# Kernel tuning notes

Hardware: AMD Instinct MI355X
Metric: run time of the kernel (lower is better)

Reference implementation:

```python
import jax, jax.numpy as jnp
import numpy as np

B, L, D, H, O = 512, 256, 256, 128, 256  # batch, max_len, input_dim, hidden_dim, output_dim


def setup_inputs() -> dict:
    key = jax.random.key(0)
    ks = jax.random.split(key, 16)
    s = 0.1
    n = jax.random.normal
    return {
        "sequences": n(ks[0], (B, L, D), jnp.float32),
        "seqlens": jax.random.randint(ks[1], (B,), 1, L + 1, jnp.int32),
        # forward-direction GRU params (PyTorch layout: gates [r, z, n] stacked)
        "Wih_f": s * n(ks[2], (3 * H, D), jnp.float32),
        "Whh_f": s * n(ks[3], (3 * H, H), jnp.float32),
        "bih_f": s * n(ks[4], (3 * H,), jnp.float32),
        "bhh_f": s * n(ks[5], (3 * H,), jnp.float32),
        # backward-direction GRU params
        "Wih_b": s * n(ks[6], (3 * H, D), jnp.float32),
        "Whh_b": s * n(ks[7], (3 * H, H), jnp.float32),
        "bih_b": s * n(ks[8], (3 * H,), jnp.float32),
        "bhh_b": s * n(ks[9], (3 * H,), jnp.float32),
        # attention MLP + context vector
        "W_mlp": s * n(ks[10], (O, 2 * H), jnp.float32),
        "b_mlp": s * n(ks[11], (O,), jnp.float32),
        "ctx": s * n(ks[12], (O,), jnp.float32),
    }


def _gru(xs, mask, Wih, Whh, bih, bhh, reverse):
    """Masked GRU scan. xs: [L,B,D], mask: [L,B,1]. Returns hidden states [L,B,H]."""
    def step(h, inp):
        x_t, m_t = inp
        gx = x_t @ Wih.T + bih          # [B, 3H]
        gh = h @ Whh.T + bhh            # [B, 3H]
        xr, xz, xn = jnp.split(gx, 3, axis=-1)
        hr, hz, hn = jnp.split(gh, 3, axis=-1)
        r = jax.nn.sigmoid(xr + hr)
        z = jax.nn.sigmoid(xz + hz)
        cand = jnp.tanh(xn + r * hn)
        h_new = (1.0 - z) * cand + z * h
        h = jnp.where(m_t, h_new, h)    # hold state on padding steps
        return h, h

    h0 = jnp.zeros((xs.shape[1], Whh.shape[1]), xs.dtype)
    _, hs = jax.lax.scan(step, h0, (xs, mask), reverse=reverse)
    return hs


def reference(sequences, seqlens, Wih_f, Whh_f, bih_f, bhh_f, Wih_b, Whh_b, bih_b, bhh_b, W_mlp, b_mlp, ctx):
    mask = jnp.arange(L)[None, :] < seqlens[:, None]      # [B, L] valid-token mask
    xs = sequences.transpose(1, 0, 2)                      # [L, B, D]
    m = mask.T[:, :, None]                                 # [L, B, 1]
    hf = _gru(xs, m, Wih_f, Whh_f, bih_f, bhh_f, False)    # forward direction
    hb = _gru(xs, m, Wih_b, Whh_b, bih_b, bhh_b, True)     # backward direction
    rnn_out = jnp.concatenate([hf, hb], axis=-1).transpose(1, 0, 2)  # [B, L, 2H]
    mlp_out = jnp.tanh(rnn_out @ W_mlp.T + b_mlp)          # [B, L, O]
    scores = jnp.einsum('blo,o->bl', mlp_out, ctx)         # [B, L]
    neg = jnp.finfo(scores.dtype).min
    w = jax.nn.softmax(jnp.where(mask, scores, neg), axis=1)  # per-sequence softmax over valid positions
    return jnp.einsum('bl,blh->bh', w, rnn_out)            # [B, 2H] attention-pooled embedding
```

## Files before the change

kernel.cpp:

```cpp
#include <hip/hip_runtime.h>
#include <hip/hip_bf16.h>
#include <cstdint>
#include <cstddef>

#define BATCH 512
#define SEQL 256
#define DIN 256
#define HID 128
#define OUTD 256
#define G3 384
#define TCH 64
#define NCH 4
#define NBS 16
#define NGRPS (BATCH/NBS)
#define MTOT (BATCH*SEQL)
#define MCH  (BATCH*TCH)
#define HSPAD 136
#define NGXT 3072

typedef __attribute__((ext_vector_type(8))) short short8v;
typedef __attribute__((ext_vector_type(4))) float float4v;

__device__ __forceinline__ unsigned short f2bf_u(float x) {
  union { float f; uint32_t u; } v; v.f = x;
  uint32_t r = v.u + 0x7FFFu + ((v.u >> 16) & 1u);
  return (unsigned short)(r >> 16);
}
__device__ __forceinline__ float bfu2f(unsigned short u) {
  union { uint32_t u; float f; } v; v.u = ((uint32_t)u) << 16; return v.f;
}
__device__ __forceinline__ float fast_tanh(float x) {
  float e2 = __expf(-2.0f * x);
  return (1.0f - e2) / (1.0f + e2);
}

__global__ __launch_bounds__(256) void prep_split(
    const float* __restrict__ Wm, unsigned short* __restrict__ mhi, unsigned short* __restrict__ mlo,
    const float* __restrict__ Wf, unsigned short* __restrict__ fhi, unsigned short* __restrict__ flo,
    const float* __restrict__ Wb, unsigned short* __restrict__ bhi, unsigned short* __restrict__ blo)
{
  int gid = blockIdx.x * 256 + threadIdx.x;
  const float* src; unsigned short* hi; unsigned short* lo; int off;
  if (gid < 16384)      { src = Wm; hi = mhi; lo = mlo; off = gid * 4; }
  else if (gid < 40960) { src = Wf; hi = fhi; lo = flo; off = (gid - 16384) * 4; }
  else                  { src = Wb; hi = bhi; lo = blo; off = (gid - 40960) * 4; }
  float4 w4 = *(const float4*)&src[off];
  ushort4 h4, l4;
  h4.x = f2bf_u(w4.x); l4.x = f2bf_u(w4.x - bfu2f(h4.x));
  h4.y = f2bf_u(w4.y); l4.y = f2bf_u(w4.y - bfu2f(h4.y));
  h4.z = f2bf_u(w4.z); l4.z = f2bf_u(w4.z - bfu2f(h4.z));
  h4.w = f2bf_u(w4.w); l4.w = f2bf_u(w4.w - bfu2f(h4.w));
  *(ushort4*)&hi[off] = h4;
  *(ushort4*)&lo[off] = l4;
}

__device__ __forceinline__ void gx_tile(
    int tid, int m0, int yy,
    const float* __restrict__ X,
    const unsigned short* __restrict__ WhiF, const unsigned short* __restrict__ WloF,
    const unsigned short* __restrict__ WhiB, const unsigned short* __restrict__ WloB,
    const float* __restrict__ bf, const float* __restrict__ bb,
    unsigned short* __restrict__ bufF, unsigned short* __restrict__ bufB, int cF, int cB,
    unsigned short* Abf, unsigned short* Bhi, unsigned short* Blo)
{
  const unsigned short* Whi; const unsigned short* Wlo;
  const float* bias; unsigned short* buf; int c;
  if (yy < 6) { Whi = WhiF; Wlo = WloF; bias = bf; buf = bufF; c = cF; }
  else        { yy -= 6; Whi = WhiB; Wlo = WloB; bias = bb; buf = bufB; c = cB; }
  const int n0 = yy * 64;

  const int l  = tid & 63;
  const int w  = tid >> 6;
  const int fr = l & 15;
  const int fk = (l >> 4) * 8;

  float4v acc[2][4];
#pragma unroll
  for (int a = 0; a < 2; ++a)
#pragma unroll
    for (int nb = 0; nb < 4; ++nb) acc[a][nb] = (float4v)0.0f;

  for (int k0 = 0; k0 < DIN; k0 += 32) {
#pragma unroll
    for (int j = 0; j < 4; ++j) {
      int row = (tid >> 3) + j * 32;
      int kq  = (tid & 7) * 4;
      int r   = m0 + row;
      int b_  = r >> 6, tt = r & 63;
      int xrow = b_ * SEQL + c * TCH + tt;
      float4 x4 = *(const float4*)&X[(size_t)xrow * DIN + k0 + kq];
      ushort4 h4 = {f2bf_u(x4.x), f2bf_u(x4.y), f2bf_u(x4.z), f2bf_u(x4.w)};
      *(ushort4*)&Abf[row * 40 + kq] = h4;
    }
    {
      int half = tid & 1;
      int cc   = tid >> 1;
      int col  = cc >> 1;
      int seg  = (cc & 1) * 16;
      const unsigned short* srcw = (half ? Wlo : Whi) + (size_t)(n0 + col) * DIN + k0 + seg;
      unsigned short* dst = (half ? Blo : Bhi) + col * 40 + seg;
      *(short8v*)dst       = *(const short8v*)srcw;
      *(short8v*)(dst + 8) = *(const short8v*)(srcw + 8);
    }
    __syncthreads();

    short8v ah[2], bh[4], blv[4];
#pragma unroll
    for (int a = 0; a < 2; ++a)
      ah[a] = *(const short8v*)&Abf[(w * 32 + a * 16 + fr) * 40 + fk];
#pragma unroll
    for (int nb = 0; nb < 4; ++nb) {
      bh[nb]  = *(const short8v*)&Bhi[(nb * 16 + fr) * 40 + fk];
      blv[nb] = *(const short8v*)&Blo[(nb * 16 + fr) * 40 + fk];
    }
#pragma unroll
    for (int a = 0; a < 2; ++a)
#pragma unroll
      for (int nb = 0; nb < 4; ++nb) {
        acc[a][nb] = __builtin_amdgcn_mfma_f32_16x16x32_bf16(ah[a], bh[nb],  acc[a][nb], 0, 0, 0);
        acc[a][nb] = __builtin_amdgcn_mfma_f32_16x16x32_bf16(ah[a], blv[nb], acc[a][nb], 0, 0, 0);
      }
    __syncthreads();
  }

#pragma unroll
  for (int a = 0; a < 2; ++a)
#pragma unroll
    for (int nb = 0; nb < 4; ++nb) {
      int gate = n0 + nb * 16 + fr;
      float bv_ = bias[gate];
#pragma unroll
      for (int reg = 0; reg < 4; ++reg) {
        int r = m0 + w * 32 + a * 16 + (l >> 4) * 4 + reg;
        buf[(size_t)r * G3 + gate] = f2bf_u(acc[a][nb][reg] + bv_);
      }
    }
}

__device__ __forceinline__ void scan_block(
    int sb, int tid,
    const int* __restrict__ seqlens,
    const float* __restrict__ Whh_f, const float* __restrict__ Whh_b,
    const float* __restrict__ bhh_f, const float* __restrict__ bhh_b,
    const unsigned short* __restrict__ bufF, const unsigned short* __restrict__ bufB,
    float* __restrict__ hstate, __hip_bfloat16* __restrict__ rnn, int ci,
    unsigned short (*hsbuf)[NBS * HSPAD])
{
  const int fwd = (sb < NGRPS) ? 1 : 0;
  const int grp = fwd ? sb : (sb - NGRPS);
  const int b0  = grp * NBS;
  const int w   = tid >> 6;
  const int l   = tid & 63;
  const int col = l & 15;
  const int rq  = l >> 4;
  const int hidx = w * 16 + col;
  const float* Whh = fwd ? Whh_f : Whh_b;
  const float* bhh = fwd ? bhh_f : bhh_b;
  const unsigned short* buf = fwd ? bufF : bufB;
  const int c = fwd ? ci : (NCH - 1 - ci);

  short8v Bh[3][4], Bl[3][4];
  float bias_[3];
#pragma unroll
  for (int j = 0; j < 3; ++j) {
    const int g = j * HID + hidx;
    bias_[j] = bhh[g];
#pragma unroll
    for (int ks = 0; ks < 4; ++ks) {
      const float* p = Whh + (size_t)g * HID + ks * 32 + rq * 8;
      float4 x0 = *(const float4*)p;
      float4 x1 = *(const float4*)(p + 4);
      float v[8] = {x0.x, x0.y, x0.z, x0.w, x1.x, x1.y, x1.z, x1.w};
      short8v hi8, lo8;
#pragma unroll
      for (int e = 0; e < 8; ++e) {
        unsigned short h = f2bf_u(v[e]);
        hi8[e] = (short)h;
        lo8[e] = (short)f2bf_u(v[e] - bfu2f(h));
      }
      Bh[j][ks] = hi8; Bl[j][ks] = lo8;
    }
  }

  int len_[4];
#pragma unroll
  for (int reg = 0; reg < 4; ++reg) len_[reg] = seqlens[b0 + rq * 4 + reg];
  int gmax = 0;
  for (int nb = 0; nb < NBS; ++nb) gmax = max(gmax, seqlens[b0 + nb]);

  float* hst = hstate + ((size_t)((fwd ? 0 : 1) * NGRPS + grp)) * (NBS * HID);
  float hold[4];
#pragma unroll
  for (int reg = 0; reg < 4; ++reg) {
    int nb = rq * 4 + reg;
    hold[reg] = (ci == 0) ? 0.0f : hst[nb * HID + hidx];
    hsbuf[0][nb * HSPAD + hidx] = f2bf_u(hold[reg]);
  }
  __syncthreads();

  int nsteps = gmax - c * TCH;
  nsteps = (nsteps > TCH) ? TCH : nsteps;

  float gxc[3][4], gxn[3][4];
  if (nsteps > 0) {
    int tt0 = fwd ? 0 : (nsteps - 1);
#pragma unroll
    for (int j = 0; j < 3; ++j)
#pragma unroll
      for (int reg = 0; reg < 4; ++reg)
        gxc[j][reg] = bfu2f(buf[(size_t)((b0 + rq * 4 + reg) * TCH + tt0) * G3 + j * HID + hidx]);
  }

  int cur = 0;
  for (int ss = 0; ss < nsteps; ++ss) {
    const int tt = fwd ? ss : (nsteps - 1 - ss);
    const int t  = c * TCH + tt;

    short8v ah[4];
#pragma unroll
    for (int ks = 0; ks < 4; ++ks)
      ah[ks] = *(const short8v*)&hsbuf[cur][col * HSPAD + ks * 32 + rq * 8];

    {
      int ssn = (ss + 1 < nsteps) ? (ss + 1) : ss;
      int ttn = fwd ? ssn : (nsteps - 1 - ssn);
#pragma unroll
      for (int j = 0; j < 3; ++j)
#pragma unroll
        for (int reg = 0; reg < 4; ++reg)
          gxn[j][reg] = bfu2f(buf[(size_t)((b0 + rq * 4 + reg) * TCH + ttn) * G3 + j * HID + hidx]);
    }

    float4v acc[3];
#pragma unroll
    for (int j = 0; j < 3; ++j)
      acc[j] = (float4v){bias_[j], bias_[j], bias_[j], bias_[j]};
#pragma unroll
    for (int ks = 0; ks < 4; ++ks) {
#pragma unroll
      for (int j = 0; j < 3; ++j) {
        acc[j] = __builtin_amdgcn_mfma_f32_16x16x32_bf16(ah[ks], Bh[j][ks], acc[j], 0, 0, 0);
        acc[j] = __builtin_amdgcn_mfma_f32_16x16x32_bf16(ah[ks], Bl[j][ks], acc[j], 0, 0, 0);
      }
    }

#pragma unroll
    for (int reg = 0; reg < 4; ++reg) {
      int nb = rq * 4 + reg;
      float gr = acc[0][reg] + gxc[0][reg];
      float gz = acc[1][reg] + gxc[1][reg];
      float gn = acc[2][reg];
      float xn = gxc[2][reg];
      float r = 1.0f / (1.0f + __expf(-gr));
      float z = 1.0f / (1.0f + __expf(-gz));
      float e2 = __expf(-2.0f * (xn + r * gn));
      float cand = (1.0f - e2) / (1.0f + e2);
      float hv = (1.0f - z) * cand + z * hold[reg];
      bool act = (t < len_[reg]);
      hv = act ? hv : hold[reg];
      hold[reg] = hv;
      hsbuf[cur ^ 1][nb * HSPAD + hidx] = f2bf_u(hv);
      if (act)
        rnn[(size_t)((b0 + nb) * SEQL + t) * OUTD + (fwd ? 0 : HID) + hidx] =
            __float2bfloat16(hv);
    }
    asm volatile("s_waitcnt lgkmcnt(0)" ::: "memory");
    __builtin_amdgcn_s_barrier();
    __builtin_amdgcn_sched_barrier(0);
    cur ^= 1;

#pragma unroll
    for (int j = 0; j < 3; ++j)
#pragma unroll
      for (int reg = 0; reg < 4; ++reg) gxc[j][reg] = gxn[j][reg];
  }

#pragma unroll
  for (int reg = 0; reg < 4; ++reg)
    hst[(rq * 4 + reg) * HID + hidx] = hold[reg];
}

__global__ __launch_bounds__(256) void gx_kernel(
    const float* __restrict__ X,
    const unsigned short* __restrict__ WhiF, const unsigned short* __restrict__ WloF,
    const unsigned short* __restrict__ WhiB, const unsigned short* __restrict__ WloB,
    const float* __restrict__ bf, const float* __restrict__ bb,
    unsigned short* __restrict__ bufF, unsigned short* __restrict__ bufB, int cF, int cB)
{
  __shared__ unsigned short Abf[128 * 40];
  __shared__ unsigned short Bhi[64 * 40];
  __shared__ unsigned short Blo[64 * 40];
  gx_tile(threadIdx.x, blockIdx.x * 128, blockIdx.y, X, WhiF, WloF, WhiB, WloB,
          bf, bb, bufF, bufB, cF, cB, Abf, Bhi, Blo);
}

__global__ __launch_bounds__(512, 2) void scan_kernel(
    const int* __restrict__ seqlens,
    const float* __restrict__ Whh_f, const float* __restrict__ Whh_b,
    const float* __restrict__ bhh_f, const float* __restrict__ bhh_b,
    const unsigned short* __restrict__ bufF, const unsigned short* __restrict__ bufB,
    float* __restrict__ hstate, __hip_bfloat16* __restrict__ rnn, int ci)
{
  __shared__ unsigned short hsbuf[2][NBS * HSPAD];
  scan_block(blockIdx.x, threadIdx.x, seqlens, Whh_f, Whh_b, bhh_f, bhh_b,
             bufF, bufB, hstate, rnn, ci, hsbuf);
}

__global__ __launch_bounds__(512, 2) void fused_kernel(
    const int* __restrict__ seqlens,
    const float* __restrict__ Whh_f, const float* __restrict__ Whh_b,
    const float* __restrict__ bhh_f, const float* __restrict__ bhh_b,
    const float* __restrict__ X,
    const unsigned short* __restrict__ WhiF, const unsigned short* __restrict__ WloF,
    const unsigned short* __restrict__ WhiB, const unsigned short* __restrict__ WloB,
    const float* __restrict__ bf, const float* __restrict__ bb,
    const unsigned short* __restrict__ rdF, const unsigned short* __restrict__ rdB,
    unsigned short* __restrict__ wrF, unsigned short* __restrict__ wrB,
    float* __restrict__ hstate, __hip_bfloat16* __restrict__ rnn, int ci)
{
  __shared__ unsigned short hsbuf[2][NBS * HSPAD];
  __shared__ unsigned short AbfS[2][128 * 40];
  __shared__ unsigned short BhiS[2][64 * 40];
  __shared__ unsigned short BloS[2][64 * 40];

  if (blockIdx.x < 2 * NGRPS) {
    scan_block(blockIdx.x, threadIdx.x, seqlens, Whh_f, Whh_b, bhh_f, bhh_b,
               rdF, rdB, hstate, rnn, ci, hsbuf);
  } else {
    const int gb   = blockIdx.x - 2 * NGRPS;
    const int half = threadIdx.x >> 8;
    const int htid = threadIdx.x & 255;
    const int t0   = gb * 2 + half;
    const int m0   = (t0 & 255) * 128;
    const int yy   = t0 >> 8;
    gx_tile(htid, m0, yy, X, WhiF, WloF, WhiB, WloB, bf, bb,
            wrF, wrB, ci + 1, NCH - 2 - ci, AbfS[half], BhiS[half], BloS[half]);
  }
}

__global__ __launch_bounds__(256) void mlp_score(
    const __hip_bfloat16* __restrict__ rnn,
    const unsigned short* __restrict__ Whi, const unsigned short* __restrict__ Wlo,
    const float* __restrict__ bmlp, const float* __restrict__ ctx,
    float* __restrict__ scoresH)
{
  __shared__ unsigned short Abf[128 * 40];
  __shared__ unsigned short BhiS[128 * 40];
  __shared__ unsigned short BloS[128 * 40];

  const int tid = threadIdx.x;
  const int m0  = blockIdx.x * 128;
  const int nh  = blockIdx.y;
  const int l   = tid & 63;
  const int w   = tid >> 6;
  const int fr  = l & 15;
  const int fk  = (l >> 4) * 8;

  float bl_[8], cl_[8];
#pragma unroll
  for (int nt = 0; nt < 8; ++nt) {
    bl_[nt] = bmlp[nh * 128 + nt * 16 + fr];
    cl_[nt] = ctx[nh * 128 + nt * 16 + fr];
  }

  float4v acc[2][8];
#pragma unroll
  for (int a = 0; a < 2; ++a)
#pragma unroll
    for (int nt = 0; nt < 8; ++nt) acc[a][nt] = (float4v)0.0f;

  for (int k0 = 0; k0 < OUTD; k0 += 32) {
    {
      int row = tid >> 1;
      int kq  = (tid & 1) * 16;
      const short* src = (const short*)rnn + (size_t)(m0 + row) * OUTD + k0 + kq;
      *(short8v*)&Abf[row * 40 + kq]     = *(const short8v*)src;
      *(short8v*)&Abf[row * 40 + kq + 8] = *(const short8v*)(src + 8);
    }
#pragma unroll
    for (int j = 0; j < 2; ++j) {
      int cid  = tid * 2 + j;
      int half = cid >> 8;
      int cc   = cid & 255;
      int colx = cc >> 1;
      int seg  = (cc & 1) * 16;
      const unsigned short* srcw = (half ? Wlo : Whi) + (size_t)(nh * 128 + colx) * OUTD + k0 + seg;
      unsigned short* dst = (half ? BloS : BhiS) + colx * 40 + seg;
      *(short8v*)dst       = *(const short8v*)srcw;
      *(short8v*)(dst + 8) = *(const short8v*)(srcw + 8);
    }
    __syncthreads();

    short8v ah0 = *(const short8v*)&Abf[(w * 32 + fr) * 40 + fk];
    short8v ah1 = *(const short8v*)&Abf[(w * 32 + 16 + fr) * 40 + fk];
#pragma unroll
    for (int nt = 0; nt < 8; ++nt) {
      short8v bh = *(const short8v*)&BhiS[(nt * 16 + fr) * 40 + fk];
      short8v bv = *(const short8v*)&BloS[(nt * 16 + fr) * 40 + fk];
      acc[0][nt] = __builtin_amdgcn_mfma_f32_16x16x32_bf16(ah0, bh, acc[0][nt], 0, 0, 0);
      acc[0][nt] = __builtin_amdgcn_mfma_f32_16x16x32_bf16(ah0, bv, acc[0][nt], 0, 0, 0);
      acc[1][nt] = __builtin_amdgcn_mfma_f32_16x16x32_bf16(ah1, bh, acc[1][nt], 0, 0, 0);
      acc[1][nt] = __builtin_amdgcn_mfma_f32_16x16x32_bf16(ah1, bv, acc[1][nt], 0, 0, 0);
    }
    __syncthreads();
  }

#pragma unroll
  for (int a = 0; a < 2; ++a) {
    float p[4] = {0.f, 0.f, 0.f, 0.f};
#pragma unroll
    for (int nt = 0; nt < 8; ++nt) {
      float bv_ = bl_[nt], cv = cl_[nt];
#pragma unroll
      for (int reg = 0; reg < 4; ++reg)
        p[reg] += fast_tanh(acc[a][nt][reg] + bv_) * cv;
    }
#pragma unroll
    for (int off = 1; off < 16; off <<= 1)
#pragma unroll
      for (int reg = 0; reg < 4; ++reg) p[reg] += __shfl_xor(p[reg], off, 64);
    if (fr == 0) {
#pragma unroll
      for (int reg = 0; reg < 4; ++reg)
        scoresH[(size_t)nh * MTOT + m0 + w * 32 + a * 16 + (l >> 4) * 4 + reg] = p[reg];
    }
  }
}

__global__ __launch_bounds__(256) void softmax_pool(
    const int* __restrict__ seqlens,
    const float* __restrict__ scoresH,
    const __hip_bfloat16* __restrict__ rnn,
    float* __restrict__ out)
{
  const int b = blockIdx.x;
  const int len = seqlens[b];
  const int tid = threadIdx.x;
  __shared__ float sm[SEQL];
  __shared__ float red[8];

  float s = (tid < len)
      ? (scoresH[b * SEQL + tid] + scoresH[(size_t)MTOT + b * SEQL + tid])
      : -3.4e38f;
  float wm = s;
#pragma unroll
  for (int off = 32; off > 0; off >>= 1) wm = fmaxf(wm, __shfl_xor(wm, off, 64));
  if ((tid & 63) == 0) red[tid >> 6] = wm;
  __syncthreads();
  float bm = fmaxf(fmaxf(red[0], red[1]), fmaxf(red[2], red[3]));

  float e = (tid < len) ? expf(s - bm) : 0.0f;
  sm[tid] = e;
  float sum = e;
#pragma unroll
  for (int off = 32; off > 0; off >>= 1) sum += __shfl_xor(sum, off, 64);
  if ((tid & 63) == 0) red[4 + (tid >> 6)] = sum;
  __syncthreads();
  float inv = 1.0f / (red[4] + red[5] + red[6] + red[7]);

  float acc = 0.0f;
  for (int l = 0; l < len; ++l)
    acc += sm[l] * __bfloat162float(rnn[(size_t)(b * SEQL + l) * OUTD + tid]);
  out[b * OUTD + tid] = acc * inv;
}

extern "C" void kernel_launch(void* const* d_in, const int* in_sizes, int n_in,
                              void* d_out, int out_size, void* d_ws, size_t ws_size,
                              hipStream_t stream) {
  const float* seq    = (const float*)d_in[0];
  const int*   lens   = (const int*)d_in[1];
  const float* Wih_f  = (const float*)d_in[2];
  const float* Whh_f  = (const float*)d_in[3];
  const float* bih_f  = (const float*)d_in[4];
  const float* bhh_f  = (const float*)d_in[5];
  const float* Wih_b  = (const float*)d_in[6];
  const float* Whh_b  = (const float*)d_in[7];
  const float* bih_b  = (const float*)d_in[8];
  const float* bhh_b  = (const float*)d_in[9];
  const float* Wmlp   = (const float*)d_in[10];
  const float* bmlp   = (const float*)d_in[11];
  const float* ctx    = (const float*)d_in[12];
  float* out = (float*)d_out;

  const size_t BUFSZ = (size_t)MCH * G3;
  const size_t needOverlap =
      4 * BUFSZ * 2 + (size_t)MTOT * OUTD * 2 + 2 * (size_t)MTOT * 4 +
      2 * BATCH * HID * 4 + 2 * (size_t)OUTD * OUTD * 2 + 4 * (size_t)G3 * DIN * 2;
  const bool overlap = (ws_size >= needOverlap);

  unsigned short* buf0F = (unsigned short*)d_ws;
  unsigned short* buf0B = buf0F + BUFSZ;
  unsigned short* buf1F = overlap ? (buf0B + BUFSZ) : buf0F;
  unsigned short* buf1B = overlap ? (buf1F + BUFSZ) : buf0B;
  unsigned short* tail  = overlap ? (buf1B + BUFSZ) : (buf0B + BUFSZ);

  __hip_bfloat16* rnn  = (__hip_bfloat16*)tail;
  float* scoresH = (float*)((unsigned short*)rnn + (size_t)MTOT * OUTD);
  float* hstate  = scoresH + 2 * (size_t)MTOT;
  unsigned short* mhi = (unsigned short*)(hstate + 2 * BATCH * HID);
  unsigned short* mlo = mhi + OUTD * OUTD;
  unsigned short* fhi = mlo + OUTD * OUTD;
  unsigned short* flo = fhi + G3 * DIN;
  unsigned short* bhi2 = flo + G3 * DIN;
  unsigned short* blo2 = bhi2 + G3 * DIN;

  prep_split<<<dim3(256), 256, 0, stream>>>(Wmlp, mhi, mlo, Wih_f, fhi, flo, Wih_b, bhi2, blo2);

  if (overlap) {
    unsigned short* bp[2][2] = {{buf0F, buf0B}, {buf1F, buf1B}};
    gx_kernel<<<dim3(256, 12), 256, 0, stream>>>(seq, fhi, flo, bhi2, blo2, bih_f, bih_b,
                                                 bp[0][0], bp[0][1], 0, NCH - 1);
    for (int k = 0; k < NCH - 1; ++k) {
      fused_kernel<<<dim3(2 * NGRPS + NGXT / 2), 512, 0, stream>>>(
          lens, Whh_f, Whh_b, bhh_f, bhh_b,
          seq, fhi, flo, bhi2, blo2, bih_f, bih_b,
          bp[k & 1][0], bp[k & 1][1], bp[(k + 1) & 1][0], bp[(k + 1) & 1][1],
          hstate, rnn, k);
    }
    scan_kernel<<<dim3(2 * NGRPS), 512, 0, stream>>>(
        lens, Whh_f, Whh_b, bhh_f, bhh_b,
        bp[(NCH - 1) & 1][0], bp[(NCH - 1) & 1][1], hstate, rnn, NCH - 1);
  } else {
    for (int ci = 0; ci < NCH; ++ci) {
      gx_kernel<<<dim3(256, 12), 256, 0, stream>>>(seq, fhi, flo, bhi2, blo2, bih_f, bih_b,
                                                   buf0F, buf0B, ci, NCH - 1 - ci);
      scan_kernel<<<dim3(2 * NGRPS), 512, 0, stream>>>(
          lens, Whh_f, Whh_b, bhh_f, bhh_b, buf0F, buf0B, hstate, rnn, ci);
    }
  }

  mlp_score<<<dim3(MTOT / 128, 2), 256, 0, stream>>>(rnn, mhi, mlo, bmlp, ctx, scoresH);
  softmax_pool<<<dim3(BATCH), 256, 0, stream>>>(lens, scoresH, rnn, out);
}
```

Measured before the change: 565.1 us.

## Overlap MLP scoring of finished timesteps with final scan chunk; split MFMA accumulators

The final scan chunk now runs in a fused kernel whose extra blocks compute MLP attention scores for timesteps 64..191. The middle chunks are already complete for both directions at that point, so their scoring overlaps the serial recurrence. A separate kernel afterward scores only the first and last 64 timesteps of each sequence. The recurrent step also accumulates the hi and lo bf16 weight halves into separate accumulators, which shortens the MFMA dependency chain on the critical path. The cost is more kernels and code, and the co-resident MLP blocks may compete with scan blocks for CU resources.

```diff
diff --git a/kernel.cpp b/kernel.cpp
--- a/kernel.cpp
+++ b/kernel.cpp
@@ -231,18 +231,22 @@
           gxn[j][reg] = bfu2f(buf[(size_t)((b0 + rq * 4 + reg) * TCH + ttn) * G3 + j * HID + hidx]);
     }
 
-    float4v acc[3];
-#pragma unroll
-    for (int j = 0; j < 3; ++j)
-      acc[j] = (float4v){bias_[j], bias_[j], bias_[j], bias_[j]};
+    float4v acc[3], accl[3];
+#pragma unroll
+    for (int j = 0; j < 3; ++j) {
+      acc[j]  = (float4v){bias_[j], bias_[j], bias_[j], bias_[j]};
+      accl[j] = (float4v)0.0f;
+    }
 #pragma unroll
     for (int ks = 0; ks < 4; ++ks) {
 #pragma unroll
       for (int j = 0; j < 3; ++j) {
-        acc[j] = __builtin_amdgcn_mfma_f32_16x16x32_bf16(ah[ks], Bh[j][ks], acc[j], 0, 0, 0);
-        acc[j] = __builtin_amdgcn_mfma_f32_16x16x32_bf16(ah[ks], Bl[j][ks], acc[j], 0, 0, 0);
+        acc[j]  = __builtin_amdgcn_mfma_f32_16x16x32_bf16(ah[ks], Bh[j][ks], acc[j],  0, 0, 0);
+        accl[j] = __builtin_amdgcn_mfma_f32_16x16x32_bf16(ah[ks], Bl[j][ks], accl[j], 0, 0, 0);
       }
     }
+#pragma unroll
+    for (int j = 0; j < 3; ++j) acc[j] += accl[j];
 
 #pragma unroll
     for (int reg = 0; reg < 4; ++reg) {
@@ -280,6 +284,81 @@
     hst[(rq * 4 + reg) * HID + hidx] = hold[reg];
 }
 
+__device__ __forceinline__ void mlp64_tile(
+    int tid, int m0, int nh,
+    const __hip_bfloat16* __restrict__ rnn,
+    const unsigned short* __restrict__ Whi, const unsigned short* __restrict__ Wlo,
+    const float* __restrict__ bmlp, const float* __restrict__ ctx,
+    float* __restrict__ scoresH,
+    unsigned short* Abf, unsigned short* BhiS, unsigned short* BloS)
+{
+  const int l  = tid & 63;
+  const int w  = tid >> 6;
+  const int fr = l & 15;
+  const int fk = (l >> 4) * 8;
+
+  float bl_[8], cl_[8];
+#pragma unroll
+  for (int nt = 0; nt < 8; ++nt) {
+    bl_[nt] = bmlp[nh * 128 + nt * 16 + fr];
+    cl_[nt] = ctx[nh * 128 + nt * 16 + fr];
+  }
+
+  float4v acc[8];
+#pragma unroll
+  for (int nt = 0; nt < 8; ++nt) acc[nt] = (float4v)0.0f;
+
+  for (int k0 = 0; k0 < OUTD; k0 += 32) {
+    {
+      int row = tid >> 2;
+      int kq  = (tid & 3) * 8;
+      *(short8v*)&Abf[row * 40 + kq] =
+          *(const short8v*)((const short*)rnn + (size_t)(m0 + row) * OUTD + k0 + kq);
+    }
+#pragma unroll
+    for (int j = 0; j < 2; ++j) {
+      int cid  = tid * 2 + j;
+      int half = cid >> 8;
+      int cc   = cid & 255;
+      int colx = cc >> 1;
+      int seg  = (cc & 1) * 16;
+      const unsigned short* srcw = (half ? Wlo : Whi) + (size_t)(nh * 128 + colx) * OUTD + k0 + seg;
+      unsigned short* dst = (half ? BloS : BhiS) + colx * 40 + seg;
+      *(short8v*)dst       = *(const short8v*)srcw;
+      *(short8v*)(dst + 8) = *(const short8v*)(srcw + 8);
+    }
+    __syncthreads();
+
+    short8v a = *(const short8v*)&Abf[(w * 16 + fr) * 40 + fk];
+#pragma unroll
+    for (int nt = 0; nt < 8; ++nt) {
+      short8v bh = *(const short8v*)&BhiS[(nt * 16 + fr) * 40 + fk];
+      short8v bv = *(const short8v*)&BloS[(nt * 16 + fr) * 40 + fk];
+      acc[nt] = __builtin_amdgcn_mfma_f32_16x16x32_bf16(a, bh, acc[nt], 0, 0, 0);
+      acc[nt] = __builtin_amdgcn_mfma_f32_16x16x32_bf16(a, bv, acc[nt], 0, 0, 0);
+    }
+    __syncthreads();
+  }
+
+  float p[4] = {0.f, 0.f, 0.f, 0.f};
+#pragma unroll
+  for (int nt = 0; nt < 8; ++nt) {
+    float bv_ = bl_[nt], cv = cl_[nt];
+#pragma unroll
+    for (int reg = 0; reg < 4; ++reg)
+      p[reg] += fast_tanh(acc[nt][reg] + bv_) * cv;
+  }
+#pragma unroll
+  for (int off = 1; off < 16; off <<= 1)
+#pragma unroll
+    for (int reg = 0; reg < 4; ++reg) p[reg] += __shfl_xor(p[reg], off, 64);
+  if (fr == 0) {
+#pragma unroll
+    for (int reg = 0; reg < 4; ++reg)
+      scoresH[(size_t)nh * MTOT + m0 + w * 16 + (l >> 4) * 4 + reg] = p[reg];
+  }
+}
+
 __global__ __launch_bounds__(256) void gx_kernel(
     const float* __restrict__ X,
     const unsigned short* __restrict__ WhiF, const unsigned short* __restrict__ WloF,
@@ -338,6 +417,39 @@
   }
 }
 
+union ShFinal {
+  unsigned short hs[2][NBS * HSPAD];
+  struct { unsigned short A[2][64 * 40]; unsigned short Bh[2][128 * 40]; unsigned short Bl[2][128 * 40]; } m;
+};
+__global__ __launch_bounds__(512, 2) void fused_final(
+    const int* __restrict__ seqlens,
+    const float* __restrict__ Whh_f, const float* __restrict__ Whh_b,
+    const float* __restrict__ bhh_f, const float* __restrict__ bhh_b,
+    const unsigned short* __restrict__ rdF, const unsigned short* __restrict__ rdB,
+    float* __restrict__ hstate, __hip_bfloat16* __restrict__ rnn,
+    const unsigned short* __restrict__ mhi, const unsigned short* __restrict__ mlo,
+    const float* __restrict__ bmlp, const float* __restrict__ ctx,
+    float* __restrict__ scoresH)
+{
+  __shared__ ShFinal sh;
+  if (blockIdx.x < 2 * NGRPS) {
+    scan_block(blockIdx.x, threadIdx.x, seqlens, Whh_f, Whh_b, bhh_f, bhh_b,
+               rdF, rdB, hstate, rnn, NCH - 1, sh.hs);
+  } else {
+    const int gb   = blockIdx.x - 2 * NGRPS;
+    const int half = threadIdx.x >> 8;
+    const int htid = threadIdx.x & 255;
+    const int body = gb * 2 + half;
+    const int nh   = body & 1;
+    const int tile = body >> 1;
+    const int b    = tile >> 1;
+    const int t0   = 64 + (tile & 1) * 64;
+    const int m0   = b * SEQL + t0;
+    mlp64_tile(htid, m0, nh, rnn, mhi, mlo, bmlp, ctx, scoresH,
+               sh.m.A[half], sh.m.Bh[half], sh.m.Bl[half]);
+  }
+}
+
 __global__ __launch_bounds__(256) void mlp_score(
     const __hip_bfloat16* __restrict__ rnn,
     const unsigned short* __restrict__ Whi, const unsigned short* __restrict__ Wlo,
@@ -423,6 +535,99 @@
 #pragma unroll
       for (int reg = 0; reg < 4; ++reg)
         scoresH[(size_t)nh * MTOT + m0 + w * 32 + a * 16 + (l >> 4) * 4 + reg] = p[reg];
+    }
+  }
+}
+
+__global__ __launch_bounds__(256) void mlp_score_rest(
+    const __hip_bfloat16* __restrict__ rnn,
+    const unsigned short* __restrict__ Whi, const unsigned short* __restrict__ Wlo,
+    const float* __restrict__ bmlp, const float* __restrict__ ctx,
+    float* __restrict__ scoresH)
+{
+  __shared__ unsigned short Abf[128 * 40];
+  __shared__ unsigned short BhiS[128 * 40];
+  __shared__ unsigned short BloS[128 * 40];
+
+  const int tid = threadIdx.x;
+  const int b   = blockIdx.x;
+  const int nh  = blockIdx.y;
+  const int l   = tid & 63;
+  const int w   = tid >> 6;
+  const int fr  = l & 15;
+  const int fk  = (l >> 4) * 8;
+
+  float bl_[8], cl_[8];
+#pragma unroll
+  for (int nt = 0; nt < 8; ++nt) {
+    bl_[nt] = bmlp[nh * 128 + nt * 16 + fr];
+    cl_[nt] = ctx[nh * 128 + nt * 16 + fr];
+  }
+
+  float4v acc[2][8];
+#pragma unroll
+  for (int a = 0; a < 2; ++a)
+#pragma unroll
+    for (int nt = 0; nt < 8; ++nt) acc[a][nt] = (float4v)0.0f;
+
+  for (int k0 = 0; k0 < OUTD; k0 += 32) {
+    {
+      int row = tid >> 1;
+      int kq  = (tid & 1) * 16;
+      int t   = (row < 64) ? row : (row + 128);
+      const short* src = (const short*)rnn + (size_t)(b * SEQL + t) * OUTD + k0 + kq;
+      *(short8v*)&Abf[row * 40 + kq]     = *(const short8v*)src;
+      *(short8v*)&Abf[row * 40 + kq + 8] = *(const short8v*)(src + 8);
+    }
+#pragma unroll
+    for (int j = 0; j < 2; ++j) {
+      int cid  = tid * 2 + j;
+      int half = cid >> 8;
+      int cc   = cid & 255;
+      int colx = cc >> 1;
+      int seg  = (cc & 1) * 16;
+      const unsigned short* srcw = (half ? Wlo : Whi) + (size_t)(nh * 128 + colx) * OUTD + k0 + seg;
+      unsigned short* dst = (half ? BloS : BhiS) + colx * 40 + seg;
+      *(short8v*)dst       = *(const short8v*)srcw;
+      *(short8v*)(dst + 8) = *(const short8v*)(srcw + 8);
+    }
+    __syncthreads();
+
+    short8v ah0 = *(const short8v*)&Abf[(w * 32 + fr) * 40 + fk];
+    short8v ah1 = *(const short8v*)&Abf[(w * 32 + 16 + fr) * 40 + fk];
+#pragma unroll
+    for (int nt = 0; nt < 8; ++nt) {
+      short8v bh = *(const short8v*)&BhiS[(nt * 16 + fr) * 40 + fk];
+      short8v bv = *(const short8v*)&BloS[(nt * 16 + fr) * 40 + fk];
+      acc[0][nt] = __builtin_amdgcn_mfma_f32_16x16x32_bf16(ah0, bh, acc[0][nt], 0, 0, 0);
+      acc[0][nt] = __builtin_amdgcn_mfma_f32_16x16x32_bf16(ah0, bv, acc[0][nt], 0, 0, 0);
+      acc[1][nt] = __builtin_amdgcn_mfma_f32_16x16x32_bf16(ah1, bh, acc[1][nt], 0, 0, 0);
+      acc[1][nt] = __builtin_amdgcn_mfma_f32_16x16x32_bf16(ah1, bv, acc[1][nt], 0, 0, 0);
+    }
+    __syncthreads();
+  }
+
+#pragma unroll
+  for (int a = 0; a < 2; ++a) {
+    float p[4] = {0.f, 0.f, 0.f, 0.f};
+#pragma unroll
+    for (int nt = 0; nt < 8; ++nt) {
+      float bv_ = bl_[nt], cv = cl_[nt];
+#pragma unroll
+      for (int reg = 0; reg < 4; ++reg)
+        p[reg] += fast_tanh(acc[a][nt][reg] + bv_) * cv;
+    }
+#pragma unroll
+    for (int off = 1; off < 16; off <<= 1)
+#pragma unroll
+      for (int reg = 0; reg < 4; ++reg) p[reg] += __shfl_xor(p[reg], off, 64);
+    if (fr == 0) {
+#pragma unroll
+      for (int reg = 0; reg < 4; ++reg) {
+        int rr = w * 32 + a * 16 + (l >> 4) * 4 + reg;
+        int t  = (rr < 64) ? rr : (rr + 128);
+        scoresH[(size_t)nh * MTOT + b * SEQL + t] = p[reg];
+      }
     }
   }
 }
@@ -517,9 +722,11 @@
           bp[k & 1][0], bp[k & 1][1], bp[(k + 1) & 1][0], bp[(k + 1) & 1][1],
           hstate, rnn, k);
     }
-    scan_kernel<<<dim3(2 * NGRPS), 512, 0, stream>>>(
+    fused_final<<<dim3(2 * NGRPS + 1024), 512, 0, stream>>>(
         lens, Whh_f, Whh_b, bhh_f, bhh_b,
-        bp[(NCH - 1) & 1][0], bp[(NCH - 1) & 1][1], hstate, rnn, NCH - 1);
+        bp[(NCH - 1) & 1][0], bp[(NCH - 1) & 1][1], hstate, rnn,
+        mhi, mlo, bmlp, ctx, scoresH);
+    mlp_score_rest<<<dim3(512, 2), 256, 0, stream>>>(rnn, mhi, mlo, bmlp, ctx, scoresH);
   } else {
     for (int ci = 0; ci < NCH; ++ci) {
       gx_kernel<<<dim3(256, 12), 256, 0, stream>>>(seq, fhi, flo, bhi2, blo2, bih_f, bih_b,
@@ -527,8 +734,8 @@
       scan_kernel<<<dim3(2 * NGRPS), 512, 0, stream>>>(
           lens, Whh_f, Whh_b, bhh_f, bhh_b, buf0F, buf0B, hstate, rnn, ci);
     }
-  }
-
-  mlp_score<<<dim3(MTOT / 128, 2), 256, 0, stream>>>(rnn, mhi, mlo, bmlp, ctx, scoresH);
+    mlp_score<<<dim3(MTOT / 128, 2), 256, 0, stream>>>(rnn, mhi, mlo, bmlp, ctx, scoresH);
+  }
+
   softmax_pool<<<dim3(BATCH), 256, 0, stream>>>(lens, scoresH, rnn, out);
 }
```

After: 539.0 us. 4.6% less time.
